# Kernel optimization log

Measured on AMD Instinct MI355X. Metric: run time of the kernel, lower is better.

## Reference

```python
import jax, jax.numpy as jnp
import numpy as np

TEMPERATURE = 0.5
N, D = 8192, 512
NUM_CLASSES = 1000


def setup_inputs() -> dict:
    key = jax.random.key(0)
    k0, k1, k2 = jax.random.split(key, 3)
    out0 = jax.random.normal(k0, (N, D), dtype=jnp.float32)
    out1 = jax.random.normal(k1, (N, D), dtype=jnp.float32)
    labels = jax.random.randint(k2, (N,), 0, NUM_CLASSES, dtype=jnp.int64)
    return {"out0": out0, "out1": out1, "labels": labels}


def _l2_normalize(x, eps=1e-12):
    # matches torch F.normalize(dim=1): x / max(||x||, eps)
    norm = jnp.sqrt(jnp.sum(x * x, axis=1, keepdims=True))
    return x / jnp.maximum(norm, eps)


def reference(out0, out1, labels):
    out0 = _l2_normalize(out0)
    out1 = _l2_normalize(out1)
    logits = jnp.matmul(out0, out1.T) / TEMPERATURE          # [N, N]
    logits_exp = jnp.exp(logits)                             # [N, N]
    positive_mask = (labels[:, None] == labels[None, :])     # [N, N] bool
    pos_sum = jnp.sum(jnp.where(positive_mask, logits_exp, 0.0), axis=1)  # [N]
    all_sum = jnp.sum(logits_exp, axis=1)                    # [N]
    loss = -jnp.mean(jnp.log(pos_sum / all_sum))
    return loss
```

## Files before the change

### kernel.cpp

```cpp
#include <hip/hip_runtime.h>

using f32x16 = __attribute__((ext_vector_type(16))) float;
using i32x8  = __attribute__((ext_vector_type(8))) int;

constexpr int   N = 8192;
constexpr int   D = 512;
constexpr float SCALE_FOLD = 1.6986436f;
constexpr int   CGROUPS = 64;

#if __has_builtin(__builtin_amdgcn_exp2f)
#define EXP2(x) __builtin_amdgcn_exp2f(x)
#else
static __device__ __forceinline__ float EXP2(float x) {
  float r;
  asm("v_exp_f32 %0, %1" : "=v"(r) : "v"(x));
  return r;
}
#endif

static __device__ __forceinline__ void gld16(const unsigned char* g, unsigned char* l) {
  __builtin_amdgcn_global_load_lds(
      (const __attribute__((address_space(1))) void*)g,
      (__attribute__((address_space(3))) void*)l, 16, 0, 0);
}

__global__ __launch_bounds__(256) void normalize_kernel(
    const float* __restrict__ in0, const float* __restrict__ in1,
    unsigned char* __restrict__ n0, unsigned char* __restrict__ n1) {
  int gw   = (blockIdx.x * 256 + threadIdx.x) >> 6;
  int lane = threadIdx.x & 63;
  int row  = (gw < N) ? gw : gw - N;
  const float* src = (gw < N) ? in0 + (size_t)row * D : in1 + (size_t)row * D;
  unsigned char* dstrow = (gw < N) ? n0 + (size_t)row * D : n1 + (size_t)row * D;

  const float4* s4 = reinterpret_cast<const float4*>(src) + (size_t)lane * 2;
  float4 v0 = s4[0], v1 = s4[1];
  float ss = v0.x*v0.x + v0.y*v0.y + v0.z*v0.z + v0.w*v0.w
           + v1.x*v1.x + v1.y*v1.y + v1.z*v1.z + v1.w*v1.w;
#pragma unroll
  for (int m = 1; m <= 32; m <<= 1) ss += __shfl_xor(ss, m);
  float s = SCALE_FOLD / fmaxf(sqrtf(ss), 1e-12f);

  int w0 = 0, w1 = 0;
  w0 = __builtin_amdgcn_cvt_pk_fp8_f32(v0.x * s, v0.y * s, w0, false);
  w0 = __builtin_amdgcn_cvt_pk_fp8_f32(v0.z * s, v0.w * s, w0, true);
  w1 = __builtin_amdgcn_cvt_pk_fp8_f32(v1.x * s, v1.y * s, w1, false);
  w1 = __builtin_amdgcn_cvt_pk_fp8_f32(v1.z * s, v1.w * s, w1, true);
  int2 o; o.x = w0; o.y = w1;

  const int c  = (row >> 1) & 3;
  const int k8 = lane & 7;
  const int g  = k8 >> 1, h = k8 & 1;
  const int off = (lane >> 3) * 64 + ((g ^ c) * 16) + h * 8;
  *reinterpret_cast<int2*>(dstrow + off) = o;
}

__global__ __launch_bounds__(256, 4) void ntxent_main(
    const unsigned char* __restrict__ n0, const unsigned char* __restrict__ n1,
    const int* __restrict__ labels,
    float* __restrict__ part_pos, float* __restrict__ part_all) {
  __shared__ unsigned char As[2][128 * 64];
  __shared__ unsigned char Bs[2][128 * 64];
  __shared__ float redS[256];
  __shared__ int   labC[128];

  const int t    = threadIdx.x;
  const int lane = t & 63;
  const int wid  = t >> 6;
  const int l31  = lane & 31;
  const int hi   = lane >> 5;
  const int wr   = wid >> 1;
  const int wc   = wid & 1;

  const int xcd = blockIdx.x & 7;
  const int c   = blockIdx.x >> 3;
  const int rowtile = (xcd >> 1) * 16 + (c & 15);
  const int colgrp  = (xcd & 1) * 32 + (c >> 4);
  const int rowbase = rowtile * 128;
  const int colb    = colgrp * 128;

  if (t < 128) labC[t] = labels[colb + t];

  const unsigned char* gA = n0 + (size_t)(rowbase + (t >> 2)) * D + (t & 3) * 16;
  const unsigned char* gB = n1 + (size_t)(colb    + (t >> 2)) * D + (t & 3) * 16;
  unsigned char* const lA = &As[0][0] + (t >> 2) * 64 + (t & 3) * 16;
  unsigned char* const lB = &Bs[0][0] + (t >> 2) * 64 + (t & 3) * 16;

#define STAGE(st, sb) do { \
    const unsigned char* _ga = gA + (st) * 64; \
    const unsigned char* _gb = gB + (st) * 64; \
    unsigned char* _la = lA + (sb) * 8192; \
    unsigned char* _lb = lB + (sb) * 8192; \
    gld16(_ga, _la); gld16(_ga + (size_t)64 * D, _la + 4096); \
    gld16(_gb, _lb); gld16(_gb + (size_t)64 * D, _lb + 4096); \
  } while (0)

  int aoff[2], boff[2];
#pragma unroll
  for (int mi = 0; mi < 2; ++mi) {
    int tr = wr * 64 + mi * 32 + l31;
    aoff[mi] = tr * 64 + (((hi << 1) ^ ((tr >> 1) & 3)) << 4);
  }
#pragma unroll
  for (int ji = 0; ji < 2; ++ji) {
    int tc = wc * 64 + ji * 32 + l31;
    boff[ji] = tc * 64 + (((hi << 1) ^ ((tc >> 1) & 3)) << 4);
  }

#define GATE4 asm volatile("s_waitcnt vmcnt(4)\n\ts_barrier" ::: "memory")
#define GATE0 asm volatile("s_waitcnt vmcnt(0)\n\ts_barrier" ::: "memory")
#define BARP  asm volatile("s_barrier" ::: "memory")
#define EBAR  asm volatile("s_waitcnt lgkmcnt(0)\n\ts_barrier" ::: "memory")

  const int sc1 = 0x7f7f7f7f;

  f32x16 acc[2][2];
#pragma unroll
  for (int ji = 0; ji < 2; ++ji)
#pragma unroll
    for (int mi = 0; mi < 2; ++mi) acc[ji][mi] = 0.f;

  STAGE(0, 0);
  STAGE(1, 1);

#pragma unroll
  for (int kk = 0; kk < 8; ++kk) {
    if (kk < 7) { GATE4; } else { GATE0; }

    const unsigned char* bufA = &As[kk & 1][0];
    const unsigned char* bufB = &Bs[kk & 1][0];
    i32x8 a[2], b[2];
#pragma unroll
    for (int mi = 0; mi < 2; ++mi) {
      int4* pa = (int4*)&a[mi];
      pa[0] = *(const int4*)&bufA[aoff[mi]];
      pa[1] = *(const int4*)&bufA[aoff[mi] ^ 16];
    }
#pragma unroll
    for (int ji = 0; ji < 2; ++ji) {
      int4* pb = (int4*)&b[ji];
      pb[0] = *(const int4*)&bufB[boff[ji]];
      pb[1] = *(const int4*)&bufB[boff[ji] ^ 16];
    }

    __builtin_amdgcn_s_setprio(1);
#pragma unroll
    for (int ji = 0; ji < 2; ++ji)
#pragma unroll
      for (int mi = 0; mi < 2; ++mi)
        acc[ji][mi] = __builtin_amdgcn_mfma_scale_f32_32x32x64_f8f6f4(
            b[ji], a[mi], acc[ji][mi], 0, 0, 0, sc1, 0, sc1);
    __builtin_amdgcn_s_setprio(0);

    if (kk < 6) { BARP; STAGE(kk + 2, kk & 1); }
  }

  int labi[2];
#pragma unroll
  for (int mi = 0; mi < 2; ++mi)
    labi[mi] = labels[rowbase + wr * 64 + mi * 32 + l31];

  float asum[2] = {0.f, 0.f};
  float psum[2] = {0.f, 0.f};
#pragma unroll
  for (int ji = 0; ji < 2; ++ji)
#pragma unroll
    for (int rq = 0; rq < 4; ++rq) {
      const int4 labj = *(const int4*)&labC[wc * 64 + ji * 32 + rq * 8 + 4 * hi];
#pragma unroll
      for (int mi = 0; mi < 2; ++mi)
#pragma unroll
        for (int rr = 0; rr < 4; ++rr) {
          float e = EXP2(acc[ji][mi][rq * 4 + rr]);
          asum[mi] += e;
          int lb = (rr == 0) ? labj.x : (rr == 1) ? labj.y : (rr == 2) ? labj.z : labj.w;
          if (lb == labi[mi]) psum[mi] += e;
        }
    }

#pragma unroll
  for (int mi = 0; mi < 2; ++mi) {
    asum[mi] += __shfl_xor(asum[mi], 32);
    psum[mi] += __shfl_xor(psum[mi], 32);
  }

  float* redSa = redS;
  float* redSp = redS + 128;
  if (wc == 1 && hi == 0) {
#pragma unroll
    for (int mi = 0; mi < 2; ++mi) {
      redSa[wr * 64 + mi * 32 + l31] = asum[mi];
      redSp[wr * 64 + mi * 32 + l31] = psum[mi];
    }
  }
  EBAR;
  if (wc == 0 && hi == 0) {
#pragma unroll
    for (int mi = 0; mi < 2; ++mi) {
      const int idx = wr * 64 + mi * 32 + l31;
      const int row = rowbase + idx;
      part_all[(size_t)colgrp * N + row] = asum[mi] + redSa[idx];
      part_pos[(size_t)colgrp * N + row] = psum[mi] + redSp[idx];
    }
  }
}

__global__ __launch_bounds__(256) void row_reduce(
    const float* __restrict__ part_pos, const float* __restrict__ part_all,
    float* __restrict__ blocksum) {
  const int i = blockIdx.x * 256 + threadIdx.x;
  float a = 0.f, p = 0.f;
#pragma unroll 4
  for (int cs = 0; cs < CGROUPS; ++cs) {
    a += part_all[(size_t)cs * N + i];
    p += part_pos[(size_t)cs * N + i];
  }
  float s = logf(a) - logf(p);
  __shared__ float red[256];
  red[threadIdx.x] = s;
  __syncthreads();
  for (int off = 128; off > 0; off >>= 1) {
    if (threadIdx.x < off) red[threadIdx.x] += red[threadIdx.x + off];
    __syncthreads();
  }
  if (threadIdx.x == 0) blocksum[blockIdx.x] = red[0];
}

__global__ __launch_bounds__(64) void final_sum(
    const float* __restrict__ blocksum, float* __restrict__ out) {
  float s = (threadIdx.x < N / 256) ? blocksum[threadIdx.x] : 0.f;
#pragma unroll
  for (int m = 1; m <= 32; m <<= 1) s += __shfl_xor(s, m);
  if (threadIdx.x == 0) out[0] = s / (float)N;
}

extern "C" void kernel_launch(void* const* d_in, const int* in_sizes, int n_in,
                              void* d_out, int out_size, void* d_ws, size_t ws_size,
                              hipStream_t stream) {
  const float* out0   = (const float*)d_in[0];
  const float* out1   = (const float*)d_in[1];
  const int*   labels = (const int*)d_in[2];
  float*       out    = (float*)d_out;

  char* ws = (char*)d_ws;
  unsigned char* n0 = (unsigned char*)ws;
  unsigned char* n1 = (unsigned char*)(ws + (size_t)N * D);
  float* part_pos = (float*)(ws + (size_t)2 * N * D);
  float* part_all = part_pos + (size_t)CGROUPS * N;
  float* blocksum = part_all + (size_t)CGROUPS * N;

  hipLaunchKernelGGL(normalize_kernel, dim3(2 * N / 4), dim3(256), 0, stream,
                     out0, out1, n0, n1);
  hipLaunchKernelGGL(ntxent_main, dim3(4096), dim3(256), 0, stream,
                     n0, n1, labels, part_pos, part_all);
  hipLaunchKernelGGL(row_reduce, dim3(N / 256), dim3(256), 0, stream,
                     part_pos, part_all, blocksum);
  hipLaunchKernelGGL(final_sum, dim3(1), dim3(64), 0, stream,
                     blocksum, out);
}
```

Baseline: 60.31 us.

## Fuse final sum into row reduce via last-block atomic counter; drop setprio

Merges the row_reduce and final_sum kernels into a single loss_reduce kernel. The last block to finish, found through an atomic counter, sums the per-block partials, which removes one kernel launch and its gap. A hipMemsetAsync is added to reset the counter each call, so the launch count stays the same, though a memset may be cheaper than a kernel. It also removes the s_setprio wrapping around the MFMA loop in the main kernel.

```diff
diff --git a/kernel.cpp b/kernel.cpp
--- a/kernel.cpp
+++ b/kernel.cpp
@@ -143,14 +143,12 @@
       pb[1] = *(const int4*)&bufB[boff[ji] ^ 16];
     }
 
-    __builtin_amdgcn_s_setprio(1);
 #pragma unroll
     for (int ji = 0; ji < 2; ++ji)
 #pragma unroll
       for (int mi = 0; mi < 2; ++mi)
         acc[ji][mi] = __builtin_amdgcn_mfma_scale_f32_32x32x64_f8f6f4(
             b[ji], a[mi], acc[ji][mi], 0, 0, 0, sc1, 0, sc1);
-    __builtin_amdgcn_s_setprio(0);
 
     if (kk < 6) { BARP; STAGE(kk + 2, kk & 1); }
   }
@@ -205,9 +203,10 @@
   }
 }
 
-__global__ __launch_bounds__(256) void row_reduce(
+__global__ __launch_bounds__(256) void loss_reduce(
     const float* __restrict__ part_pos, const float* __restrict__ part_all,
-    float* __restrict__ blocksum) {
+    float* __restrict__ blocksum, unsigned* __restrict__ counter,
+    float* __restrict__ out) {
   const int i = blockIdx.x * 256 + threadIdx.x;
   float a = 0.f, p = 0.f;
 #pragma unroll 4
@@ -217,21 +216,28 @@
   }
   float s = logf(a) - logf(p);
   __shared__ float red[256];
+  __shared__ unsigned done;
   red[threadIdx.x] = s;
   __syncthreads();
   for (int off = 128; off > 0; off >>= 1) {
     if (threadIdx.x < off) red[threadIdx.x] += red[threadIdx.x + off];
     __syncthreads();
   }
-  if (threadIdx.x == 0) blocksum[blockIdx.x] = red[0];
-}
-
-__global__ __launch_bounds__(64) void final_sum(
-    const float* __restrict__ blocksum, float* __restrict__ out) {
-  float s = (threadIdx.x < N / 256) ? blocksum[threadIdx.x] : 0.f;
-#pragma unroll
-  for (int m = 1; m <= 32; m <<= 1) s += __shfl_xor(s, m);
-  if (threadIdx.x == 0) out[0] = s / (float)N;
+  if (threadIdx.x == 0) {
+    blocksum[blockIdx.x] = red[0];
+    __threadfence();
+    done = atomicAdd(counter, 1u);
+  }
+  __syncthreads();
+  if (done == gridDim.x - 1) {
+    __threadfence();
+    if (threadIdx.x < 64) {
+      float v = (threadIdx.x < N / 256) ? blocksum[threadIdx.x] : 0.f;
+#pragma unroll
+      for (int m = 1; m <= 32; m <<= 1) v += __shfl_xor(v, m);
+      if (threadIdx.x == 0) out[0] = v / (float)N;
+    }
+  }
 }
 
 extern "C" void kernel_launch(void* const* d_in, const int* in_sizes, int n_in,
@@ -248,13 +254,13 @@
   float* part_pos = (float*)(ws + (size_t)2 * N * D);
   float* part_all = part_pos + (size_t)CGROUPS * N;
   float* blocksum = part_all + (size_t)CGROUPS * N;
-
+  unsigned* counter = (unsigned*)(blocksum + 32);
+
+  hipMemsetAsync(counter, 0, sizeof(unsigned), stream);
   hipLaunchKernelGGL(normalize_kernel, dim3(2 * N / 4), dim3(256), 0, stream,
                      out0, out1, n0, n1);
   hipLaunchKernelGGL(ntxent_main, dim3(4096), dim3(256), 0, stream,
                      n0, n1, labels, part_pos, part_all);
-  hipLaunchKernelGGL(row_reduce, dim3(N / 256), dim3(256), 0, stream,
-                     part_pos, part_all, blocksum);
-  hipLaunchKernelGGL(final_sum, dim3(1), dim3(64), 0, stream,
-                     blocksum, out);
-}
+  hipLaunchKernelGGL(loss_reduce, dim3(N / 256), dim3(256), 0, stream,
+                     part_pos, part_all, blocksum, counter, out);
+}
```

Result: slower. 66.54 us (+10.3%).
